# Kernel optimization log

Hardware: AMD Instinct MI355X
Metric: run time of the kernel (lower is better)

## Reference

```python
import jax, jax.numpy as jnp
import numpy as np

RADIUS = 2.0  # param['BaseScale'] in repo configs


def fps(xyz, npoint):
    """Farthest point sampling. xyz: [B,N,3] -> idx [B,npoint]."""
    B, N, _ = xyz.shape

    def step(carry, _):
        dists, last_idx = carry  # [B,N], [B]
        last = jnp.take_along_axis(xyz, last_idx[:, None, None], axis=1)  # [B,1,3]
        d = jnp.sum((xyz - last) ** 2, axis=-1)  # [B,N]
        dists = jnp.minimum(dists, d)
        nxt = jnp.argmax(dists, axis=-1).astype(jnp.int32)
        return (dists, nxt), last_idx

    init = (jnp.full((B, N), jnp.inf, xyz.dtype), jnp.zeros((B,), jnp.int32))
    _, idxs = jax.lax.scan(step, init, None, length=npoint)  # [npoint,B]
    return jnp.transpose(idxs)  # [B,npoint]


def ball_query(xyz, new_xyz, nsample, radius):
    """For each center, first `nsample` point indices within radius, padded with first hit."""
    N = xyz.shape[1]
    d2 = jnp.sum((new_xyz[:, :, None, :] - xyz[:, None, :, :]) ** 2, axis=-1)  # [B,np,N]
    key = jnp.where(d2 < radius * radius, jnp.arange(N)[None, None, :], N)  # int keys
    sk = jnp.sort(key, axis=-1)[..., :nsample]  # first hits by index order
    idx = jnp.where(sk < N, sk, sk[..., :1])  # pad with first valid index
    return jnp.minimum(idx, N - 1).astype(jnp.int32)  # center is always in-ball, so safe


def conv_bn_relu(x, w, b):
    # 1x1 Conv2D_BN: channel matmul + bias (inference BN folded as affine) + relu
    return jax.nn.relu(jnp.einsum('bpsc,cd->bpsd', x, w) + b)


def detection_forward(xyz, w0, b0, w1, b1, w2, b2, w3, b3, w4, b4,
                      att_w, att_b, ori_w, ori_b, num_clusters, num_samples):
    B = xyz.shape[0]
    fps_idx = fps(xyz, num_clusters)  # [B,np]
    new_xyz = jnp.take_along_axis(xyz, fps_idx[:, :, None], axis=1)  # [B,np,3]
    idx = ball_query(xyz, new_xyz, num_samples, RADIUS)  # [B,np,ns]
    grouped = xyz[jnp.arange(B)[:, None, None], idx]  # [B,np,ns,3]
    # translate to local frame and normalize by radius (normalize_radius=True, use_xyz=True)
    new_points = (grouped - new_xyz[:, :, None, :]) / RADIUS
    # shared MLP on each point in each cluster
    new_points = conv_bn_relu(new_points, w0, b0)
    new_points = conv_bn_relu(new_points, w1, b1)
    new_points = conv_bn_relu(new_points, w2, b2)
    # MaxPoolAxis: max over nsample axis, keepdims
    new_points = jnp.max(new_points, axis=2, keepdims=True)  # [B,np,1,256]
    # mlp2
    new_points = conv_bn_relu(new_points, w3, b3)
    new_points = conv_bn_relu(new_points, w4, b4)  # [B,np,1,64]
    # attention head: 1x1 conv + softplus, squeeze W and C axes
    attention = jax.nn.softplus(jnp.einsum('bpsc,cd->bpsd', new_points, att_w) + att_b)
    attention = attention[:, :, 0, 0]  # [B,np]
    # orientation head: 1x1 conv -> 2 ch, l2-normalize, atan2
    oxy = (jnp.einsum('bpsc,cd->bpsd', new_points, ori_w) + ori_b)[:, :, 0, :]  # [B,np,2]
    oxy = oxy / jnp.sqrt(jnp.maximum(jnp.sum(oxy * oxy, axis=2, keepdims=True), 1e-8))
    orientation = jnp.arctan2(oxy[:, :, 1], oxy[:, :, 0])  # [B,np]
    return new_xyz, idx, attention, orientation


def setup_inputs() -> dict:
    key = jax.random.key(0)
    ks = jax.random.split(key, 16)
    s = lambda k, shp, fan: jax.random.normal(k, shp, jnp.float32) * (1.0 / np.sqrt(fan))
    return {
        'xyz': jax.random.normal(ks[0], (8, 16384, 3), jnp.float32) * 20.0,  # lidar-scale coords
        'w0': s(ks[1], (3, 64), 3), 'b0': jnp.zeros((64,), jnp.float32),
        'w1': s(ks[2], (64, 128), 64), 'b1': jnp.zeros((128,), jnp.float32),
        'w2': s(ks[3], (128, 256), 128), 'b2': jnp.zeros((256,), jnp.float32),
        'w3': s(ks[4], (256, 128), 256), 'b3': jnp.zeros((128,), jnp.float32),
        'w4': s(ks[5], (128, 64), 128), 'b4': jnp.zeros((64,), jnp.float32),
        'att_w': s(ks[6], (64, 1), 64), 'att_b': jnp.zeros((1,), jnp.float32),
        'ori_w': s(ks[7], (64, 2), 64), 'ori_b': jnp.zeros((2,), jnp.float32),
        'num_clusters': 512,
        'num_samples': 64,
    }


def reference(xyz, w0, b0, w1, b1, w2, b2, w3, b3, w4, b4,
              att_w, att_b, ori_w, ori_b, num_clusters, num_samples):
    return detection_forward(xyz, w0, b0, w1, b1, w2, b2, w3, b3, w4, b4,
                             att_w, att_b, ori_w, ori_b, int(num_clusters), int(num_samples))
```

## Files before the change

### kernel.cpp

```cpp
#include <hip/hip_runtime.h>
#include <math.h>

#define B_ 8
#define N_ 16384
#define P_ 512

#define OFF_NEWXYZ 0
#define OFF_IDX    12288
#define OFF_ATT    274432
#define OFF_ORI    278528

__global__ __launch_bounds__(1024) void fps_kernel(const float* __restrict__ xyz,
                                                   float* __restrict__ out_newxyz)
{
    const int b = blockIdx.x;
    const int t = threadIdx.x;
    const int lane = t & 63;
    const int wid = t >> 6;
    const float* base = xyz + (size_t)b * N_ * 3;

    float px[16], py[16], pz[16], dd[16];
#pragma unroll
    for (int k = 0; k < 16; ++k) {
        int j = t + k * 1024;
        px[k] = base[j * 3 + 0];
        py[k] = base[j * 3 + 1];
        pz[k] = base[j * 3 + 2];
        dd[k] = __builtin_inff();
    }

    __shared__ float red_d[16];
    __shared__ int   red_i[16];
    __shared__ int   winner[2];

    float lx = base[0], ly = base[1], lz = base[2];
    if (t == 0) {
        int o = b * P_ * 3;
        out_newxyz[o + 0] = lx; out_newxyz[o + 1] = ly; out_newxyz[o + 2] = lz;
    }

    for (int p = 1; p < P_; ++p) {
        float bestd = -1.0f;
        int   besti = 0;
#pragma unroll
        for (int k = 0; k < 16; ++k) {
            float dx = __fsub_rn(px[k], lx);
            float dy = __fsub_rn(py[k], ly);
            float dz = __fsub_rn(pz[k], lz);
            float d2 = __fadd_rn(__fadd_rn(__fmul_rn(dx, dx), __fmul_rn(dy, dy)),
                                 __fmul_rn(dz, dz));
            float nd = fminf(dd[k], d2);
            dd[k] = nd;
            bool gt = nd > bestd;
            besti = gt ? (t + k * 1024) : besti;
            bestd = gt ? nd : bestd;
        }
#pragma unroll
        for (int m = 1; m < 64; m <<= 1) {
            float od = __shfl_xor(bestd, m, 64);
            int   oi = __shfl_xor(besti, m, 64);
            bool take = (od > bestd) || (od == bestd && oi < besti);
            bestd = take ? od : bestd;
            besti = take ? oi : besti;
        }
        if (lane == 0) { red_d[wid] = bestd; red_i[wid] = besti; }
        __syncthreads();
        if (t == 0) {
            float bd = red_d[0]; int bi = red_i[0];
#pragma unroll
            for (int w = 1; w < 16; ++w) {
                float d = red_d[w]; int i = red_i[w];
                if (d > bd || (d == bd && i < bi)) { bd = d; bi = i; }
            }
            winner[p & 1] = bi;
        }
        __syncthreads();
        int wi = winner[p & 1];
        lx = base[wi * 3 + 0];
        ly = base[wi * 3 + 1];
        lz = base[wi * 3 + 2];
        if (t == 0) {
            int o = (b * P_ + p) * 3;
            out_newxyz[o + 0] = lx; out_newxyz[o + 1] = ly; out_newxyz[o + 2] = lz;
        }
    }
}

__global__ __launch_bounds__(256) void mlp_kernel(
    const float* __restrict__ xyz,
    const float* __restrict__ centers,
    const float* __restrict__ w0, const float* __restrict__ b0,
    const float* __restrict__ w1, const float* __restrict__ b1,
    const float* __restrict__ w2, const float* __restrict__ b2,
    const float* __restrict__ w3, const float* __restrict__ b3,
    const float* __restrict__ w4, const float* __restrict__ b4,
    const float* __restrict__ attw, const float* __restrict__ attb,
    const float* __restrict__ oriw, const float* __restrict__ orib,
    float* __restrict__ out_idx,
    float* __restrict__ out_att,
    float* __restrict__ out_ori)
{
    const int bp = blockIdx.x;
    const int b = bp >> 9;
    const int tid = threadIdx.x;
    const int lane = tid & 63;
    const int w = tid >> 6;
    const float* base = xyz + (size_t)b * N_ * 3;

    __shared__ __attribute__((aligned(16))) float h0s[64 * 68];
    __shared__ __attribute__((aligned(16))) float h1s[64 * 132];
    __shared__ float qx[64], qy[64], qz[64];
    __shared__ float vmaxs[256];
    __shared__ float h3s[128];
    __shared__ float h4s[64];
    __shared__ int s_hits[4][64];
    __shared__ int s_cnt[4];
    __shared__ int s_sel[64];
    float* red = h0s;

    const float cx = centers[bp * 3 + 0];
    const float cy = centers[bp * 3 + 1];
    const float cz = centers[bp * 3 + 2];

    {
        const int qbase = w * 4096;
        int cnt = 0;
        for (int chunk = 0; chunk < 64 && cnt < 64; ++chunk) {
            int j = qbase + chunk * 64 + lane;
            float x = base[j * 3 + 0];
            float y = base[j * 3 + 1];
            float z = base[j * 3 + 2];
            float dx = __fsub_rn(cx, x);
            float dy = __fsub_rn(cy, y);
            float dz = __fsub_rn(cz, z);
            float d2 = __fadd_rn(__fadd_rn(__fmul_rn(dx, dx), __fmul_rn(dy, dy)),
                                 __fmul_rn(dz, dz));
            bool in = d2 < 4.0f;
            unsigned long long m = __ballot(in);
            if (in) {
                int pos = cnt + (int)__popcll(m & ((1ULL << lane) - 1ULL));
                if (pos < 64) s_hits[w][pos] = j;
            }
            cnt += (int)__popcll(m);
        }
        if (lane == 0) s_cnt[w] = cnt;
    }
    __syncthreads();
    if (tid < 64) {
        int off = 0, sel = -1;
#pragma unroll
        for (int ww = 0; ww < 4; ++ww) {
            int c = s_cnt[ww];
            int r = tid - off;
            if (sel < 0 && r >= 0 && r < c) sel = s_hits[ww][r];
            off += c;
        }
        s_sel[tid] = sel;
    }
    __syncthreads();

    if (tid < 64) {
        int sel = s_sel[tid];
        int pad = s_sel[0];
        if (sel < 0) sel = pad;
        sel = min(sel, N_ - 1);
        out_idx[bp * 64 + tid] = (float)sel;
        const float* pp = base + (size_t)sel * 3;
        qx[tid] = (pp[0] - cx) * 0.5f;
        qy[tid] = (pp[1] - cy) * 0.5f;
        qz[tid] = (pp[2] - cz) * 0.5f;
    }
    __syncthreads();

#pragma unroll
    for (int k = 0; k < 16; ++k) {
        int o = tid + k * 256;
        int s = o >> 6, d = o & 63;
        float v = b0[d] + qx[s] * w0[d] + qy[s] * w0[64 + d] + qz[s] * w0[128 + d];
        h0s[s * 68 + d] = fmaxf(v, 0.0f);
    }
    __syncthreads();

    const int ts = tid >> 4, td = tid & 15;

    {
        const int d0 = td * 8;
        float acc[4][8];
#pragma unroll
        for (int j = 0; j < 8; ++j) {
            float bv = b1[d0 + j];
#pragma unroll
            for (int r = 0; r < 4; ++r) acc[r][j] = bv;
        }
        for (int cb = 0; cb < 64; cb += 4) {
            float a[4][4];
#pragma unroll
            for (int r = 0; r < 4; ++r) {
                float4 t4 = *(const float4*)&h0s[(ts + 16 * r) * 68 + cb];
                a[r][0] = t4.x; a[r][1] = t4.y; a[r][2] = t4.z; a[r][3] = t4.w;
            }
#pragma unroll
            for (int cc = 0; cc < 4; ++cc) {
                const float* wr = w1 + (cb + cc) * 128 + d0;
                float4 wA = *(const float4*)wr;
                float4 wB = *(const float4*)(wr + 4);
                float wv[8] = {wA.x, wA.y, wA.z, wA.w, wB.x, wB.y, wB.z, wB.w};
#pragma unroll
                for (int r = 0; r < 4; ++r)
#pragma unroll
                    for (int j = 0; j < 8; ++j)
                        acc[r][j] = fmaf(a[r][cc], wv[j], acc[r][j]);
            }
        }
#pragma unroll
        for (int r = 0; r < 4; ++r)
#pragma unroll
            for (int j = 0; j < 8; ++j)
                h1s[(ts + 16 * r) * 132 + d0 + j] = fmaxf(acc[r][j], 0.0f);
    }
    __syncthreads();

    {
        const int d0 = td * 16;
        float acc[4][16];
#pragma unroll
        for (int j = 0; j < 16; ++j) {
            float bv = b2[d0 + j];
#pragma unroll
            for (int r = 0; r < 4; ++r) acc[r][j] = bv;
        }
        for (int cb = 0; cb < 128; cb += 4) {
            float a[4][4];
#pragma unroll
            for (int r = 0; r < 4; ++r) {
                float4 t4 = *(const float4*)&h1s[(ts + 16 * r) * 132 + cb];
                a[r][0] = t4.x; a[r][1] = t4.y; a[r][2] = t4.z; a[r][3] = t4.w;
            }
#pragma unroll
            for (int cc = 0; cc < 4; ++cc) {
                const float* wr = w2 + (cb + cc) * 256 + d0;
                float4 wA = *(const float4*)wr;
                float4 wB = *(const float4*)(wr + 4);
                float4 wC = *(const float4*)(wr + 8);
                float4 wD = *(const float4*)(wr + 12);
                float wv[16] = {wA.x, wA.y, wA.z, wA.w, wB.x, wB.y, wB.z, wB.w,
                                wC.x, wC.y, wC.z, wC.w, wD.x, wD.y, wD.z, wD.w};
#pragma unroll
                for (int r = 0; r < 4; ++r)
#pragma unroll
                    for (int j = 0; j < 16; ++j)
                        acc[r][j] = fmaf(a[r][cc], wv[j], acc[r][j]);
            }
        }
#pragma unroll
        for (int j = 0; j < 16; ++j) {
            float v = fmaxf(fmaxf(acc[0][j], acc[1][j]), fmaxf(acc[2][j], acc[3][j]));
            red[ts * 256 + d0 + j] = v;
        }
    }
    __syncthreads();
    {
        float m = red[tid];
#pragma unroll
        for (int ww = 1; ww < 16; ++ww) m = fmaxf(m, red[ww * 256 + tid]);
        vmaxs[tid] = fmaxf(m, 0.0f);
    }
    __syncthreads();

    if (tid < 128) {
        float acc = b3[tid];
        for (int c = 0; c < 256; ++c) acc = fmaf(vmaxs[c], w3[c * 128 + tid], acc);
        h3s[tid] = fmaxf(acc, 0.0f);
    }
    __syncthreads();
    if (tid < 64) {
        float acc = b4[tid];
        for (int c = 0; c < 128; ++c) acc = fmaf(h3s[c], w4[c * 64 + tid], acc);
        h4s[tid] = fmaxf(acc, 0.0f);
    }
    __syncthreads();
    if (tid < 64) {
        float h = h4s[tid];
        float pa  = h * attw[tid];
        float pox = h * oriw[tid * 2 + 0];
        float poy = h * oriw[tid * 2 + 1];
#pragma unroll
        for (int m = 1; m < 64; m <<= 1) {
            pa  += __shfl_xor(pa, m, 64);
            pox += __shfl_xor(pox, m, 64);
            poy += __shfl_xor(poy, m, 64);
        }
        if (tid == 0) {
            float z = pa + attb[0];
            float att = fmaxf(z, 0.0f) + log1pf(expf(-fabsf(z)));
            float ox = pox + orib[0], oy = poy + orib[1];
            float n = sqrtf(fmaxf(ox * ox + oy * oy, 1e-8f));
            ox /= n; oy /= n;
            out_att[bp] = att;
            out_ori[bp] = atan2f(oy, ox);
        }
    }
}

extern "C" void kernel_launch(void* const* d_in, const int* in_sizes, int n_in,
                              void* d_out, int out_size, void* d_ws, size_t ws_size,
                              hipStream_t stream)
{
    const float* xyz  = (const float*)d_in[0];
    const float* w0   = (const float*)d_in[1];
    const float* b0   = (const float*)d_in[2];
    const float* w1   = (const float*)d_in[3];
    const float* b1   = (const float*)d_in[4];
    const float* w2   = (const float*)d_in[5];
    const float* b2   = (const float*)d_in[6];
    const float* w3   = (const float*)d_in[7];
    const float* b3   = (const float*)d_in[8];
    const float* w4   = (const float*)d_in[9];
    const float* b4   = (const float*)d_in[10];
    const float* attw = (const float*)d_in[11];
    const float* attb = (const float*)d_in[12];
    const float* oriw = (const float*)d_in[13];
    const float* orib = (const float*)d_in[14];

    float* out = (float*)d_out;
    float* out_newxyz = out + OFF_NEWXYZ;
    float* out_idx    = out + OFF_IDX;
    float* out_att    = out + OFF_ATT;
    float* out_ori    = out + OFF_ORI;

    fps_kernel<<<dim3(B_), dim3(1024), 0, stream>>>(xyz, out_newxyz);
    mlp_kernel<<<dim3(B_ * P_), dim3(256), 0, stream>>>(
        xyz, out_newxyz,
        w0, b0, w1, b1, w2, b2, w3, b3, w4, b4,
        attw, attb, oriw, orib, out_idx, out_att, out_ori);
}
```

Before: 2.273 ms.

## Cut FPS per-iteration sync: carry winner coords, redundant final reduce, 512 threads

The FPS kernel now runs 512 threads per block, each holding 32 points, and carries the winning point's coordinates through the wave shuffle reduction. Every thread redundantly reduces the 8 per-wave results from double-buffered shared memory. This removes the second __syncthreads and the dependent global reload of the winner's coordinates on each of the 511 serial iterations. In exchange it does three extra shuffles per reduction step and uses more registers per thread.

```diff
diff --git a/kernel.cpp b/kernel.cpp
--- a/kernel.cpp
+++ b/kernel.cpp
@@ -10,8 +10,8 @@
 #define OFF_ATT    274432
 #define OFF_ORI    278528
 
-__global__ __launch_bounds__(1024) void fps_kernel(const float* __restrict__ xyz,
-                                                   float* __restrict__ out_newxyz)
+__global__ __launch_bounds__(512, 2) void fps_kernel(const float* __restrict__ xyz,
+                                                     float* __restrict__ out_newxyz)
 {
     const int b = blockIdx.x;
     const int t = threadIdx.x;
@@ -19,19 +19,18 @@
     const int wid = t >> 6;
     const float* base = xyz + (size_t)b * N_ * 3;
 
-    float px[16], py[16], pz[16], dd[16];
-#pragma unroll
-    for (int k = 0; k < 16; ++k) {
-        int j = t + k * 1024;
+    float px[32], py[32], pz[32], dd[32];
+#pragma unroll
+    for (int k = 0; k < 32; ++k) {
+        int j = t + k * 512;
         px[k] = base[j * 3 + 0];
         py[k] = base[j * 3 + 1];
         pz[k] = base[j * 3 + 2];
         dd[k] = __builtin_inff();
     }
 
-    __shared__ float red_d[16];
-    __shared__ int   red_i[16];
-    __shared__ int   winner[2];
+    __shared__ float s_d[2][8], s_x[2][8], s_y[2][8], s_z[2][8];
+    __shared__ int   s_i[2][8];
 
     float lx = base[0], ly = base[1], lz = base[2];
     if (t == 0) {
@@ -39,11 +38,13 @@
         out_newxyz[o + 0] = lx; out_newxyz[o + 1] = ly; out_newxyz[o + 2] = lz;
     }
 
+#pragma unroll 1
     for (int p = 1; p < P_; ++p) {
         float bestd = -1.0f;
-        int   besti = 0;
-#pragma unroll
-        for (int k = 0; k < 16; ++k) {
+        int   bestk = 0;
+        float bx = 0.0f, by = 0.0f, bz = 0.0f;
+#pragma unroll
+        for (int k = 0; k < 32; ++k) {
             float dx = __fsub_rn(px[k], lx);
             float dy = __fsub_rn(py[k], ly);
             float dz = __fsub_rn(pz[k], lz);
@@ -52,33 +53,44 @@
             float nd = fminf(dd[k], d2);
             dd[k] = nd;
             bool gt = nd > bestd;
-            besti = gt ? (t + k * 1024) : besti;
             bestd = gt ? nd : bestd;
-        }
+            bestk = gt ? k : bestk;
+            bx = gt ? px[k] : bx;
+            by = gt ? py[k] : by;
+            bz = gt ? pz[k] : bz;
+        }
+        int besti = t + bestk * 512;
+
 #pragma unroll
         for (int m = 1; m < 64; m <<= 1) {
             float od = __shfl_xor(bestd, m, 64);
             int   oi = __shfl_xor(besti, m, 64);
+            float ox = __shfl_xor(bx, m, 64);
+            float oy = __shfl_xor(by, m, 64);
+            float oz = __shfl_xor(bz, m, 64);
             bool take = (od > bestd) || (od == bestd && oi < besti);
             bestd = take ? od : bestd;
             besti = take ? oi : besti;
-        }
-        if (lane == 0) { red_d[wid] = bestd; red_i[wid] = besti; }
+            bx = take ? ox : bx;
+            by = take ? oy : by;
+            bz = take ? oz : bz;
+        }
+        const int pb = p & 1;
+        if (lane == 0) {
+            s_d[pb][wid] = bestd; s_i[pb][wid] = besti;
+            s_x[pb][wid] = bx;    s_y[pb][wid] = by;    s_z[pb][wid] = bz;
+        }
         __syncthreads();
-        if (t == 0) {
-            float bd = red_d[0]; int bi = red_i[0];
-#pragma unroll
-            for (int w = 1; w < 16; ++w) {
-                float d = red_d[w]; int i = red_i[w];
-                if (d > bd || (d == bd && i < bi)) { bd = d; bi = i; }
-            }
-            winner[p & 1] = bi;
-        }
-        __syncthreads();
-        int wi = winner[p & 1];
-        lx = base[wi * 3 + 0];
-        ly = base[wi * 3 + 1];
-        lz = base[wi * 3 + 2];
+        float bd = s_d[pb][0]; int bi = s_i[pb][0]; int bw = 0;
+#pragma unroll
+        for (int w = 1; w < 8; ++w) {
+            float d = s_d[pb][w]; int i = s_i[pb][w];
+            bool take = (d > bd) || (d == bd && i < bi);
+            bd = take ? d : bd;
+            bi = take ? i : bi;
+            bw = take ? w : bw;
+        }
+        lx = s_x[pb][bw]; ly = s_y[pb][bw]; lz = s_z[pb][bw];
         if (t == 0) {
             int o = (b * P_ + p) * 3;
             out_newxyz[o + 0] = lx; out_newxyz[o + 1] = ly; out_newxyz[o + 2] = lz;
@@ -328,7 +340,7 @@
     float* out_att    = out + OFF_ATT;
     float* out_ori    = out + OFF_ORI;
 
-    fps_kernel<<<dim3(B_), dim3(1024), 0, stream>>>(xyz, out_newxyz);
+    fps_kernel<<<dim3(B_), dim3(512), 0, stream>>>(xyz, out_newxyz);
     mlp_kernel<<<dim3(B_ * P_), dim3(256), 0, stream>>>(
         xyz, out_newxyz,
         w0, b0, w1, b1, w2, b2, w3, b3, w4, b4,
```

Result: faster. 2.083 ms (-8.4%).
